# Performance work log

Hardware: AMD Instinct MI355X
Metric: run time of the kernel (lower is better)

Reference implementation:

```python
import jax, jax.numpy as jnp
import numpy as np

N_EMBD = 1024
N_HEAD = 16
B, T, T_MEM = 4, 1024, 1024


def setup_inputs() -> dict:
    key = jax.random.key(0)
    ks = jax.random.split(key, 11)
    s = 1.0 / np.sqrt(N_EMBD)
    return {
        "q_in": jax.random.normal(ks[0], (B, T, N_EMBD), jnp.float32),
        "k_in": jax.random.normal(ks[1], (B, T_MEM, N_EMBD), jnp.float32),
        "v_in": jax.random.normal(ks[2], (B, T_MEM, N_EMBD), jnp.float32),
        # torch nn.Linear weights: [out_features, in_features]
        "Wq": jax.random.normal(ks[3], (N_EMBD, N_EMBD), jnp.float32) * s,
        "bq": jax.random.normal(ks[4], (N_EMBD,), jnp.float32) * s,
        "Wk": jax.random.normal(ks[5], (N_EMBD, N_EMBD), jnp.float32) * s,
        "bk": jax.random.normal(ks[6], (N_EMBD,), jnp.float32) * s,
        "Wv": jax.random.normal(ks[7], (N_EMBD, N_EMBD), jnp.float32) * s,
        "bv": jax.random.normal(ks[8], (N_EMBD,), jnp.float32) * s,
        "Wo": jax.random.normal(ks[9], (N_EMBD, N_EMBD), jnp.float32) * s,
        "bo": jax.random.normal(ks[10], (N_EMBD,), jnp.float32) * s,
    }


def reference(q_in, k_in, v_in, Wq, bq, Wk, bk, Wv, bv, Wo, bo):
    b, t, c = q_in.shape
    t_mem = k_in.shape[1]
    hd = c // N_HEAD  # head dim

    def proj(x, W, bias):
        return x @ W.T + bias

    # [b, h, t, hd]
    q = proj(q_in, Wq, bq).reshape(b, t, N_HEAD, hd).transpose(0, 2, 1, 3)
    k = proj(k_in, Wk, bk).reshape(b, t_mem, N_HEAD, hd).transpose(0, 2, 1, 3)
    v = proj(v_in, Wv, bv).reshape(b, t_mem, N_HEAD, hd).transpose(0, 2, 1, 3)

    scale = 1.0 / np.sqrt(hd).astype(np.float32)
    att = jnp.einsum("bhqd,bhkd->bhqk", q, k) * scale
    att = jax.nn.softmax(att, axis=-1)  # dropout p=0 -> identity

    y = jnp.einsum("bhqk,bhkd->bhqd", att, v)
    y = y.transpose(0, 2, 1, 3).reshape(b, t, c)
    y = proj(y, Wo, bo)  # resid_drop p=0 -> identity

    attention = jnp.mean(att, axis=1)  # mean over heads: [b, t, t_mem]
    return (y, attention)
```

## Files before the change

kernel.cpp:

```cpp
#include <hip/hip_runtime.h>
#include <hip/hip_fp16.h>


typedef __attribute__((ext_vector_type(8))) short s16x8;
typedef __attribute__((ext_vector_type(4))) float f32x4;
typedef __attribute__((ext_vector_type(4))) unsigned short u16x4;

#define N_EMBD 1024
#define NH 16
#define BT 4096
#define STR 1032

#if __has_builtin(__builtin_amdgcn_global_load_lds)
#define HAVE_GLL 1
#define GLDS16(g, l)                                                              \
  __builtin_amdgcn_global_load_lds((__attribute__((address_space(1))) void*)(g), \
                                   (__attribute__((address_space(3))) void*)(l), 16, 0, 0)
#else
#define HAVE_GLL 0
#endif

static __device__ __forceinline__ unsigned short f2bf(float f) {
  unsigned int u = __builtin_bit_cast(unsigned int, f);
  u += 0x7FFFu + ((u >> 16) & 1u);
  return (unsigned short)(u >> 16);
}
static __device__ __forceinline__ float bf2f(unsigned short h) {
  return __builtin_bit_cast(float, ((unsigned int)h) << 16);
}

__global__ __launch_bounds__(256) void cvt_in3(const float* __restrict__ q,
                                               const float* __restrict__ k,
                                               const float* __restrict__ v,
                                               unsigned short* __restrict__ out) {
  const int z = blockIdx.z;
  const float* src = (z == 0) ? q : (z == 1 ? k : v);
  int i = (blockIdx.x * 256 + threadIdx.x) * 4;
  float4 val = *(const float4*)(src + i);
  u16x4 o;
  o[0] = f2bf(val.x);
  o[1] = f2bf(val.y);
  o[2] = f2bf(val.z);
  o[3] = f2bf(val.w);
  *(u16x4*)(out + (size_t)z * BT * N_EMBD + i) = o;
}

__global__ __launch_bounds__(256) void cvt_w4(const float* __restrict__ wo,
                                              const float* __restrict__ wq,
                                              const float* __restrict__ wk,
                                              const float* __restrict__ wv,
                                              unsigned short* __restrict__ out) {
  const int z = blockIdx.z;
  const float* src = (z == 0) ? wo : (z == 1 ? wq : (z == 2 ? wk : wv));
  const float scale = (z == 1) ? 0.125f : 1.0f;
  int i = (blockIdx.x * 256 + threadIdx.x) * 4;
  float4 val = *(const float4*)(src + i);
  u16x4 o;
  o[0] = f2bf(val.x * scale);
  o[1] = f2bf(val.y * scale);
  o[2] = f2bf(val.z * scale);
  o[3] = f2bf(val.w * scale);
  *(u16x4*)(out + (size_t)z * N_EMBD * N_EMBD + i) = o;
}

template <bool F32OUT>
static __device__ __forceinline__ void gemm_bt_tile(const unsigned short* __restrict__ A,
                                                    const unsigned short* __restrict__ B,
                                                    const float* __restrict__ bias, float bscale,
                                                    void* __restrict__ Cout,
                                                    int m0, int n0, int N, int K,
                                                    unsigned short* Al, unsigned short* Bl) {
  const int tid = threadIdx.x;
  const int l = tid & 63, w = tid >> 6;
  const int wr = w >> 1, wc = w & 1;
  const int l15 = l & 15, l4 = l >> 4;
  const int srow = tid >> 3;
  const int skk = (tid & 7) * 8;
  f32x4 acc[4][4] = {};
  for (int k0 = 0; k0 < K; k0 += 64) {
#if HAVE_GLL
#pragma unroll
    for (int i = 0; i < 4; ++i) {
      GLDS16(&A[(size_t)(m0 + i * 32 + srow) * K + k0 + skk], Al + i * 2048 + w * 512);
      GLDS16(&B[(size_t)(n0 + i * 32 + srow) * K + k0 + skk], Bl + i * 2048 + w * 512);
    }
#else
#pragma unroll
    for (int i = 0; i < 4; ++i) {
      int row = i * 32 + srow;
      *(s16x8*)&Al[row * 64 + skk] = *(const s16x8*)&A[(size_t)(m0 + row) * K + k0 + skk];
      *(s16x8*)&Bl[row * 64 + skk] = *(const s16x8*)&B[(size_t)(n0 + row) * K + k0 + skk];
    }
#endif
    __syncthreads();
#pragma unroll
    for (int kf = 0; kf < 2; ++kf) {
      s16x8 af[4], bfr[4];
#pragma unroll
      for (int mi = 0; mi < 4; ++mi)
        af[mi] = *(const s16x8*)&Al[(wr * 64 + mi * 16 + l15) * 64 + kf * 32 + l4 * 8];
#pragma unroll
      for (int nj = 0; nj < 4; ++nj)
        bfr[nj] = *(const s16x8*)&Bl[(wc * 64 + nj * 16 + l15) * 64 + kf * 32 + l4 * 8];
#pragma unroll
      for (int mi = 0; mi < 4; ++mi) {
#pragma unroll
        for (int nj = 0; nj < 4; ++nj)
          acc[mi][nj] =
              __builtin_amdgcn_mfma_f32_16x16x32_bf16(af[mi], bfr[nj], acc[mi][nj], 0, 0, 0);
      }
    }
    __syncthreads();
  }
#pragma unroll
  for (int nj = 0; nj < 4; ++nj) {
    int col = n0 + wc * 64 + nj * 16 + l15;
    float bv = bias[col] * bscale;
#pragma unroll
    for (int mi = 0; mi < 4; ++mi) {
#pragma unroll
      for (int r = 0; r < 4; ++r) {
        int row = m0 + wr * 64 + mi * 16 + l4 * 4 + r;
        float v = acc[mi][nj][r] + bv;
        if constexpr (F32OUT)
          ((float*)Cout)[(size_t)row * N + col] = v;
        else
          ((unsigned short*)Cout)[(size_t)row * N + col] = f2bf(v);
      }
    }
  }
}

__global__ __launch_bounds__(256) void gemm_qkv(const unsigned short* __restrict__ Xin,
                                                const unsigned short* __restrict__ Wbf,
                                                const float* __restrict__ bq,
                                                const float* __restrict__ bk,
                                                const float* __restrict__ bv,
                                                unsigned short* __restrict__ Cout) {
  __shared__ unsigned short Al[128 * 64];
  __shared__ unsigned short Bl[128 * 64];
  const int z = blockIdx.z;
  const float* bias = (z == 0) ? bq : (z == 1 ? bk : bv);
  const float bscale = (z == 0) ? 0.125f : 1.0f;
  gemm_bt_tile<false>(Xin + (size_t)z * BT * N_EMBD,
                      Wbf + (size_t)(1 + z) * N_EMBD * N_EMBD, bias, bscale,
                      Cout + (size_t)z * BT * N_EMBD, blockIdx.x * 128, blockIdx.y * 128,
                      N_EMBD, N_EMBD, Al, Bl);
}

__global__ __launch_bounds__(256) void gemm_out(const unsigned short* __restrict__ Ybf,
                                                const unsigned short* __restrict__ Wo,
                                                const float* __restrict__ bo,
                                                float* __restrict__ Cout) {
  __shared__ unsigned short Al[128 * 64];
  __shared__ unsigned short Bl[128 * 64];
  gemm_bt_tile<true>(Ybf, Wo, bo, 1.0f, Cout, blockIdx.x * 128, blockIdx.y * 128, N_EMBD, N_EMBD,
                     Al, Bl);
}

__global__ __launch_bounds__(256) void transpose_v(const unsigned short* __restrict__ Vp,
                                                   unsigned short* __restrict__ Vt) {
  __shared__ unsigned short tile[64][65];
  const int t0 = blockIdx.x * 64, h = blockIdx.y, b = blockIdx.z;
  const int r = threadIdx.x >> 2, c0 = (threadIdx.x & 3) * 16;
  const unsigned short* src = Vp + (size_t)(b * 1024 + t0 + r) * 1024 + h * 64 + c0;
#pragma unroll
  for (int j = 0; j < 16; ++j) tile[r][c0 + j] = src[j];
  __syncthreads();
  unsigned short* dst = Vt + (size_t)((b * 16 + h) * 64 + r) * 1024 + t0 + c0;
#pragma unroll
  for (int j = 0; j < 16; ++j) dst[j] = tile[c0 + j][r];
}

__global__ __launch_bounds__(512, 4) void attn_ph2(const unsigned short* __restrict__ Qp,
                                                   const unsigned short* __restrict__ Kp,
                                                   const unsigned short* __restrict__ Vt,
                                                   unsigned short* __restrict__ Ybf,
                                                   unsigned short* __restrict__ Pmean) {
  __shared__ __align__(16) unsigned short S2[2][16 * STR];
  __shared__ float RedM[2][16][4];
  __shared__ float RedS[2][16][4];
  const int tid = threadIdx.x;
  const int tm = tid >> 8;
  const int ttid = tid & 255;
  const int w4 = ttid >> 6;
  const int l = tid & 63;
  const int l15 = l & 15, l4 = l >> 4;
  const int r = ttid & 15, c = ttid >> 4;

  int bid = blockIdx.x;
  int swz = (bid & 7) * 64 + (bid >> 3);
  int qt = swz & 63;
  int grp = swz >> 6;
  int b = grp >> 1, hg = grp & 1;
  int q0 = qt * 16;

  __half2 am[32];
#pragma unroll
  for (int j = 0; j < 32; ++j) am[j] = __float2half2_rn(0.f);

#pragma unroll 1
  for (int it = 0; it < 4; ++it) {
    const int h = hg * 8 + it * 2 + tm;
    const unsigned short* qbase = Qp + (size_t)(b * 1024 + q0 + l15) * 1024 + h * 64 + l4 * 8;
    s16x8 aq0 = *(const s16x8*)qbase;
    s16x8 aq1 = *(const s16x8*)(qbase + 32);
    float m = -3.4e38f;
#pragma unroll
    for (int nt = 0; nt < 16; ++nt) {
      int gn = w4 * 16 + nt;
      const unsigned short* kb = Kp + (size_t)(b * 1024 + gn * 16 + l15) * 1024 + h * 64 + l4 * 8;
      f32x4 s = {};
      s = __builtin_amdgcn_mfma_f32_16x16x32_bf16(*(const s16x8*)kb, aq0, s, 0, 0, 0);
      s = __builtin_amdgcn_mfma_f32_16x16x32_bf16(*(const s16x8*)(kb + 32), aq1, s, 0, 0, 0);
      u16x4 pk;
#pragma unroll
      for (int rr = 0; rr < 4; ++rr) {
        m = fmaxf(m, s[rr]);
        pk[rr] = f2bf(s[rr]);
      }
      *(u16x4*)&S2[tm][l15 * STR + gn * 16 + l4 * 4] = pk;
    }
    m = fmaxf(m, __shfl_xor(m, 16));
    m = fmaxf(m, __shfl_xor(m, 32));
    if (l < 16) RedM[tm][l][w4] = m;
    __syncthreads();

    float mm = fmaxf(fmaxf(RedM[tm][r][0], RedM[tm][r][1]),
                     fmaxf(RedM[tm][r][2], RedM[tm][r][3]));
    float ps = 0.f;
#pragma unroll
    for (int k = 0; k < 8; ++k) {
      unsigned short* sp = &S2[tm][r * STR + c * 64 + k * 8];
      s16x8 sv = *(const s16x8*)sp;
      s16x8 pv;
#pragma unroll
      for (int j = 0; j < 8; ++j) {
        float e = __expf(bf2f((unsigned short)sv[j]) - mm);
        ps += e;
        pv[j] = (short)f2bf(e);
      }
      *(s16x8*)sp = pv;
    }
    ps += __shfl_xor(ps, 16);
    ps += __shfl_xor(ps, 32);
    if (l < 16) RedS[tm][l][w4] = ps;
    __syncthreads();

    float lsA = RedS[tm][l15][0] + RedS[tm][l15][1] + RedS[tm][l15][2] + RedS[tm][l15][3];
    float fac = 0.0625f / lsA;
    f32x4 y = {};
    const unsigned short* vb = Vt + (size_t)((b * 16 + h) * 64 + w4 * 16 + l15) * 1024 + l4 * 8;
#pragma unroll
    for (int kq = 0; kq < 4; ++kq) {
#pragma unroll
      for (int kk = 0; kk < 8; ++kk) {
        const int ks = kq * 8 + kk;
        s16x8 pa = *(const s16x8*)&S2[tm][l15 * STR + ks * 32 + l4 * 8];
        y = __builtin_amdgcn_mfma_f32_16x16x32_bf16(pa, *(const s16x8*)(vb + ks * 32), y, 0, 0, 0);
        if (kq == w4) {
#pragma unroll
          for (int e2 = 0; e2 < 4; ++e2) {
            float2 fv;
            fv.x = bf2f((unsigned short)pa[e2 * 2]) * fac;
            fv.y = bf2f((unsigned short)pa[e2 * 2 + 1]) * fac;
            am[kk * 4 + e2] = __hadd2(am[kk * 4 + e2], __float22half2_rn(fv));
          }
        }
      }
    }
#pragma unroll
    for (int rr = 0; rr < 4; ++rr) {
      int row = l4 * 4 + rr;
      float lsr = RedS[tm][row][0] + RedS[tm][row][1] + RedS[tm][row][2] + RedS[tm][row][3];
      Ybf[(size_t)(b * 1024 + q0 + row) * 1024 + h * 64 + w4 * 16 + l15] = f2bf(y[rr] / lsr);
    }
    __syncthreads();
  }

  unsigned int* us = (unsigned int*)S2;
  if (tm == 1) {
#pragma unroll
    for (int j = 0; j < 32; ++j) us[ttid * 32 + j] = __builtin_bit_cast(unsigned int, am[j]);
  }
  __syncthreads();
  if (tm == 0) {
    unsigned short* pm =
        Pmean + (size_t)((b * 2 + hg) * 1024 + q0 + l15) * 1024 + w4 * 256 + l4 * 8;
#pragma unroll
    for (int kk = 0; kk < 8; ++kk) {
      s16x8 ov;
#pragma unroll
      for (int e2 = 0; e2 < 4; ++e2) {
        int j = kk * 4 + e2;
        __half2 ot = __builtin_bit_cast(__half2, us[ttid * 32 + j]);
        float2 fo = __half22float2(ot);
        float2 fm = __half22float2(am[j]);
        ov[e2 * 2] = (short)f2bf(fm.x + fo.x);
        ov[e2 * 2 + 1] = (short)f2bf(fm.y + fo.y);
      }
      *(s16x8*)&pm[kk * 32] = ov;
    }
  }
}

__global__ __launch_bounds__(256) void mean2(const unsigned short* __restrict__ P2,
                                             float* __restrict__ out) {
  size_t f = ((size_t)blockIdx.x * 256 + threadIdx.x) * 8;
  int b = (int)(f >> 20);
  size_t i0 = f + ((size_t)b << 20);
  s16x8 a = *(const s16x8*)&P2[i0];
  s16x8 d = *(const s16x8*)&P2[i0 + (1u << 20)];
  float4 o0, o1;
  o0.x = bf2f((unsigned short)a[0]) + bf2f((unsigned short)d[0]);
  o0.y = bf2f((unsigned short)a[1]) + bf2f((unsigned short)d[1]);
  o0.z = bf2f((unsigned short)a[2]) + bf2f((unsigned short)d[2]);
  o0.w = bf2f((unsigned short)a[3]) + bf2f((unsigned short)d[3]);
  o1.x = bf2f((unsigned short)a[4]) + bf2f((unsigned short)d[4]);
  o1.y = bf2f((unsigned short)a[5]) + bf2f((unsigned short)d[5]);
  o1.z = bf2f((unsigned short)a[6]) + bf2f((unsigned short)d[6]);
  o1.w = bf2f((unsigned short)a[7]) + bf2f((unsigned short)d[7]);
  *(float4*)&out[f] = o0;
  *(float4*)&out[f + 4] = o1;
}

extern "C" void kernel_launch(void* const* d_in, const int* in_sizes, int n_in, void* d_out,
                              int out_size, void* d_ws, size_t ws_size, hipStream_t stream) {
  const float* q_in = (const float*)d_in[0];
  const float* k_in = (const float*)d_in[1];
  const float* v_in = (const float*)d_in[2];
  const float* Wq = (const float*)d_in[3];
  const float* bq = (const float*)d_in[4];
  const float* Wk = (const float*)d_in[5];
  const float* bk = (const float*)d_in[6];
  const float* Wv = (const float*)d_in[7];
  const float* bv = (const float*)d_in[8];
  const float* Wo = (const float*)d_in[9];
  const float* bo = (const float*)d_in[10];

  float* out_y = (float*)d_out;
  float* out_att = out_y + (size_t)BT * N_EMBD;

  char* ws = (char*)d_ws;
  const size_t MB = 1024 * 1024;
  unsigned short* xin_bf = (unsigned short*)(ws);
  unsigned short* W_bf = (unsigned short*)(ws + 24 * MB);
  unsigned short* Qp = (unsigned short*)(ws + 32 * MB);
  unsigned short* Kp = Qp + (size_t)BT * N_EMBD;
  unsigned short* Vp = Kp + (size_t)BT * N_EMBD;
  unsigned short* Pmean = (unsigned short*)(ws);
  unsigned short* Vt = (unsigned short*)(ws + 16 * MB);
  unsigned short* Ybf = Vp;

  const int NIN = BT * N_EMBD;
  const int NW = N_EMBD * N_EMBD;

  cvt_in3<<<dim3(NIN / 1024, 1, 3), 256, 0, stream>>>(q_in, k_in, v_in, xin_bf);
  cvt_w4<<<dim3(NW / 1024, 1, 4), 256, 0, stream>>>(Wo, Wq, Wk, Wv, W_bf);

  gemm_qkv<<<dim3(BT / 128, N_EMBD / 128, 3), 256, 0, stream>>>(xin_bf, W_bf, bq, bk, bv, Qp);
  transpose_v<<<dim3(16, 16, 4), 256, 0, stream>>>(Vp, Vt);
  attn_ph2<<<512, 512, 0, stream>>>(Qp, Kp, Vt, Ybf, Pmean);
  mean2<<<2048, 256, 0, stream>>>(Pmean, out_att);
  gemm_out<<<dim3(BT / 128, N_EMBD / 128), 256, 0, stream>>>(Ybf, W_bf, bo, out_y);
}
```

Measured before the change: 232.4 us.

## Double attention query tile to 32 rows per block with 1024-thread blocks

The attention kernel now processes 32 query rows per block instead of 16. Each loaded K fragment is reused for two query sub-tiles, and the block grows to 1024 threads with half as many blocks. This is meant to halve K global traffic per query row and amortise Q/K loads. In exchange the S2 scratch doubles to about 132 KB of LDS, which can limit occupancy to one block per CU. The grid shrinks to 256 blocks, and the block-index swizzle is replaced by a simpler mapping.

```diff
diff --git a/kernel.cpp b/kernel.cpp
--- a/kernel.cpp
+++ b/kernel.cpp
@@ -172,28 +172,28 @@
   for (int j = 0; j < 16; ++j) dst[j] = tile[c0 + j][r];
 }
 
-__global__ __launch_bounds__(512, 4) void attn_ph2(const unsigned short* __restrict__ Qp,
-                                                   const unsigned short* __restrict__ Kp,
-                                                   const unsigned short* __restrict__ Vt,
-                                                   unsigned short* __restrict__ Ybf,
-                                                   unsigned short* __restrict__ Pmean) {
-  __shared__ __align__(16) unsigned short S2[2][16 * STR];
-  __shared__ float RedM[2][16][4];
-  __shared__ float RedS[2][16][4];
+__global__ __launch_bounds__(1024, 4) void attn_ph2(const unsigned short* __restrict__ Qp,
+                                                    const unsigned short* __restrict__ Kp,
+                                                    const unsigned short* __restrict__ Vt,
+                                                    unsigned short* __restrict__ Ybf,
+                                                    unsigned short* __restrict__ Pmean) {
+  __shared__ __align__(16) unsigned short S2[2][32 * STR];
+  __shared__ float RedM[2][32][8];
+  __shared__ float RedS[2][32][8];
   const int tid = threadIdx.x;
-  const int tm = tid >> 8;
-  const int ttid = tid & 255;
+  const int tm = tid >> 9;
+  const int ttid = tid & 511;
   const int w4 = ttid >> 6;
   const int l = tid & 63;
   const int l15 = l & 15, l4 = l >> 4;
-  const int r = ttid & 15, c = ttid >> 4;
-
-  int bid = blockIdx.x;
-  int swz = (bid & 7) * 64 + (bid >> 3);
-  int qt = swz & 63;
-  int grp = swz >> 6;
-  int b = grp >> 1, hg = grp & 1;
-  int q0 = qt * 16;
+  const int r = ttid & 31, c = ttid >> 5;
+  const int qgw = w4 >> 2;
+  const int dtw = w4 & 3;
+
+  const int bid = blockIdx.x;
+  const int grp = bid & 7, qt = bid >> 3;
+  const int b = grp >> 1, hg = grp & 1;
+  const int q0 = qt * 32;
 
   __half2 am[32];
 #pragma unroll
@@ -202,32 +202,48 @@
 #pragma unroll 1
   for (int it = 0; it < 4; ++it) {
     const int h = hg * 8 + it * 2 + tm;
-    const unsigned short* qbase = Qp + (size_t)(b * 1024 + q0 + l15) * 1024 + h * 64 + l4 * 8;
-    s16x8 aq0 = *(const s16x8*)qbase;
-    s16x8 aq1 = *(const s16x8*)(qbase + 32);
-    float m = -3.4e38f;
-#pragma unroll
-    for (int nt = 0; nt < 16; ++nt) {
-      int gn = w4 * 16 + nt;
+    const unsigned short* qb0 = Qp + (size_t)(b * 1024 + q0 + l15) * 1024 + h * 64 + l4 * 8;
+    const unsigned short* qb1 = qb0 + (size_t)16 * 1024;
+    s16x8 aq00 = *(const s16x8*)qb0;
+    s16x8 aq01 = *(const s16x8*)(qb0 + 32);
+    s16x8 aq10 = *(const s16x8*)qb1;
+    s16x8 aq11 = *(const s16x8*)(qb1 + 32);
+    float m0 = -3.4e38f, m1 = -3.4e38f;
+#pragma unroll
+    for (int nt = 0; nt < 8; ++nt) {
+      int gn = w4 * 8 + nt;
       const unsigned short* kb = Kp + (size_t)(b * 1024 + gn * 16 + l15) * 1024 + h * 64 + l4 * 8;
-      f32x4 s = {};
-      s = __builtin_amdgcn_mfma_f32_16x16x32_bf16(*(const s16x8*)kb, aq0, s, 0, 0, 0);
-      s = __builtin_amdgcn_mfma_f32_16x16x32_bf16(*(const s16x8*)(kb + 32), aq1, s, 0, 0, 0);
-      u16x4 pk;
+      s16x8 kf0 = *(const s16x8*)kb;
+      s16x8 kf1 = *(const s16x8*)(kb + 32);
+      f32x4 s0 = {}, s1 = {};
+      s0 = __builtin_amdgcn_mfma_f32_16x16x32_bf16(kf0, aq00, s0, 0, 0, 0);
+      s0 = __builtin_amdgcn_mfma_f32_16x16x32_bf16(kf1, aq01, s0, 0, 0, 0);
+      s1 = __builtin_amdgcn_mfma_f32_16x16x32_bf16(kf0, aq10, s1, 0, 0, 0);
+      s1 = __builtin_amdgcn_mfma_f32_16x16x32_bf16(kf1, aq11, s1, 0, 0, 0);
+      u16x4 p0, p1;
 #pragma unroll
       for (int rr = 0; rr < 4; ++rr) {
-        m = fmaxf(m, s[rr]);
-        pk[rr] = f2bf(s[rr]);
-      }
-      *(u16x4*)&S2[tm][l15 * STR + gn * 16 + l4 * 4] = pk;
-    }
-    m = fmaxf(m, __shfl_xor(m, 16));
-    m = fmaxf(m, __shfl_xor(m, 32));
-    if (l < 16) RedM[tm][l][w4] = m;
-    __syncthreads();
-
-    float mm = fmaxf(fmaxf(RedM[tm][r][0], RedM[tm][r][1]),
-                     fmaxf(RedM[tm][r][2], RedM[tm][r][3]));
+        m0 = fmaxf(m0, s0[rr]);
+        p0[rr] = f2bf(s0[rr]);
+        m1 = fmaxf(m1, s1[rr]);
+        p1[rr] = f2bf(s1[rr]);
+      }
+      *(u16x4*)&S2[tm][l15 * STR + gn * 16 + l4 * 4] = p0;
+      *(u16x4*)&S2[tm][(16 + l15) * STR + gn * 16 + l4 * 4] = p1;
+    }
+    m0 = fmaxf(m0, __shfl_xor(m0, 16));
+    m0 = fmaxf(m0, __shfl_xor(m0, 32));
+    m1 = fmaxf(m1, __shfl_xor(m1, 16));
+    m1 = fmaxf(m1, __shfl_xor(m1, 32));
+    if (l < 16) {
+      RedM[tm][l][w4] = m0;
+      RedM[tm][16 + l][w4] = m1;
+    }
+    __syncthreads();
+
+    float mm = RedM[tm][r][0];
+#pragma unroll
+    for (int j = 1; j < 8; ++j) mm = fmaxf(mm, RedM[tm][r][j]);
     float ps = 0.f;
 #pragma unroll
     for (int k = 0; k < 8; ++k) {
@@ -242,23 +258,25 @@
       }
       *(s16x8*)sp = pv;
     }
-    ps += __shfl_xor(ps, 16);
     ps += __shfl_xor(ps, 32);
-    if (l < 16) RedS[tm][l][w4] = ps;
-    __syncthreads();
-
-    float lsA = RedS[tm][l15][0] + RedS[tm][l15][1] + RedS[tm][l15][2] + RedS[tm][l15][3];
+    if (l < 32) RedS[tm][l][w4] = ps;
+    __syncthreads();
+
+    float lsA = 0.f;
+#pragma unroll
+    for (int j = 0; j < 8; ++j) lsA += RedS[tm][qgw * 16 + l15][j];
     float fac = 0.0625f / lsA;
     f32x4 y = {};
-    const unsigned short* vb = Vt + (size_t)((b * 16 + h) * 64 + w4 * 16 + l15) * 1024 + l4 * 8;
+    const unsigned short* vb =
+        Vt + (size_t)((b * 16 + h) * 64 + dtw * 16 + l15) * 1024 + l4 * 8;
 #pragma unroll
     for (int kq = 0; kq < 4; ++kq) {
 #pragma unroll
       for (int kk = 0; kk < 8; ++kk) {
         const int ks = kq * 8 + kk;
-        s16x8 pa = *(const s16x8*)&S2[tm][l15 * STR + ks * 32 + l4 * 8];
+        s16x8 pa = *(const s16x8*)&S2[tm][(qgw * 16 + l15) * STR + ks * 32 + l4 * 8];
         y = __builtin_amdgcn_mfma_f32_16x16x32_bf16(pa, *(const s16x8*)(vb + ks * 32), y, 0, 0, 0);
-        if (kq == w4) {
+        if (kq == dtw) {
 #pragma unroll
           for (int e2 = 0; e2 < 4; ++e2) {
             float2 fv;
@@ -271,9 +289,11 @@
     }
 #pragma unroll
     for (int rr = 0; rr < 4; ++rr) {
-      int row = l4 * 4 + rr;
-      float lsr = RedS[tm][row][0] + RedS[tm][row][1] + RedS[tm][row][2] + RedS[tm][row][3];
-      Ybf[(size_t)(b * 1024 + q0 + row) * 1024 + h * 64 + w4 * 16 + l15] = f2bf(y[rr] / lsr);
+      int row = qgw * 16 + l4 * 4 + rr;
+      float lsr = 0.f;
+#pragma unroll
+      for (int j = 0; j < 8; ++j) lsr += RedS[tm][row][j];
+      Ybf[(size_t)(b * 1024 + q0 + row) * 1024 + h * 64 + dtw * 16 + l15] = f2bf(y[rr] / lsr);
     }
     __syncthreads();
   }
@@ -285,8 +305,8 @@
   }
   __syncthreads();
   if (tm == 0) {
-    unsigned short* pm =
-        Pmean + (size_t)((b * 2 + hg) * 1024 + q0 + l15) * 1024 + w4 * 256 + l4 * 8;
+    unsigned short* pm = Pmean + ((size_t)(b * 2 + hg) << 20) +
+                         (size_t)(q0 + qgw * 16 + l15) * 1024 + dtw * 256 + l4 * 8;
 #pragma unroll
     for (int kk = 0; kk < 8; ++kk) {
       s16x8 ov;
@@ -360,7 +380,7 @@
 
   gemm_qkv<<<dim3(BT / 128, N_EMBD / 128, 3), 256, 0, stream>>>(xin_bf, W_bf, bq, bk, bv, Qp);
   transpose_v<<<dim3(16, 16, 4), 256, 0, stream>>>(Vp, Vt);
-  attn_ph2<<<512, 512, 0, stream>>>(Qp, Kp, Vt, Ybf, Pmean);
+  attn_ph2<<<256, 1024, 0, stream>>>(Qp, Kp, Vt, Ybf, Pmean);
   mean2<<<2048, 256, 0, stream>>>(Pmean, out_att);
   gemm_out<<<dim3(BT / 128, N_EMBD / 128), 256, 0, stream>>>(Ybf, W_bf, bo, out_y);
 }
```

Result: faster. 222.2 us (-4.4%).

## Double attention query tile per block and keep scores in registers before softmax

Applied to the files above, without the earlier changes.

The attention kernel now handles 32 query rows per block with 1024 threads instead of 16 rows with 512, halving the grid. Each wave keeps its QK^T scores in registers, takes the row max, then exponentiates and writes bf16 probabilities to shared memory only once. This removes the bf16 round trip of raw scores through LDS and packs with v_cvt_pk_bf16_f32. It also raises wave priority around the MFMA loops. The costs are a larger LDS footprint and more register pressure per block, fewer blocks per CU, and a dropped block-index swizzle that may change L2 locality.

```diff
diff --git a/kernel.cpp b/kernel.cpp
--- a/kernel.cpp
+++ b/kernel.cpp
@@ -172,28 +172,29 @@
   for (int j = 0; j < 16; ++j) dst[j] = tile[c0 + j][r];
 }
 
-__global__ __launch_bounds__(512, 4) void attn_ph2(const unsigned short* __restrict__ Qp,
-                                                   const unsigned short* __restrict__ Kp,
-                                                   const unsigned short* __restrict__ Vt,
-                                                   unsigned short* __restrict__ Ybf,
-                                                   unsigned short* __restrict__ Pmean) {
-  __shared__ __align__(16) unsigned short S2[2][16 * STR];
-  __shared__ float RedM[2][16][4];
-  __shared__ float RedS[2][16][4];
+__global__ __launch_bounds__(1024, 4) void attn_ph2(const unsigned short* __restrict__ Qp,
+                                                    const unsigned short* __restrict__ Kp,
+                                                    const unsigned short* __restrict__ Vt,
+                                                    unsigned short* __restrict__ Ybf,
+                                                    unsigned short* __restrict__ Pmean) {
+  __shared__ __align__(16) unsigned short S2[2][32 * STR];
+  __shared__ float RedM[2][32][8];
+  __shared__ float RedS[2][32][4];
   const int tid = threadIdx.x;
-  const int tm = tid >> 8;
-  const int ttid = tid & 255;
+  const int tm = tid >> 9;
+  const int ttid = tid & 511;
   const int w4 = ttid >> 6;
   const int l = tid & 63;
   const int l15 = l & 15, l4 = l >> 4;
-  const int r = ttid & 15, c = ttid >> 4;
-
-  int bid = blockIdx.x;
-  int swz = (bid & 7) * 64 + (bid >> 3);
-  int qt = swz & 63;
-  int grp = swz >> 6;
-  int b = grp >> 1, hg = grp & 1;
-  int q0 = qt * 16;
+  const int qg = w4 & 1;
+  const int gnr = w4 >> 1;
+  const int qgw = w4 >> 2;
+  const int dtw = w4 & 3;
+
+  const int bid = blockIdx.x;
+  const int grp = bid & 7, qt = bid >> 3;
+  const int b = grp >> 1, hg = grp & 1;
+  const int q0 = qt * 32;
 
   __half2 am[32];
 #pragma unroll
@@ -202,63 +203,70 @@
 #pragma unroll 1
   for (int it = 0; it < 4; ++it) {
     const int h = hg * 8 + it * 2 + tm;
-    const unsigned short* qbase = Qp + (size_t)(b * 1024 + q0 + l15) * 1024 + h * 64 + l4 * 8;
+    const unsigned short* qbase =
+        Qp + (size_t)(b * 1024 + q0 + qg * 16 + l15) * 1024 + h * 64 + l4 * 8;
     s16x8 aq0 = *(const s16x8*)qbase;
     s16x8 aq1 = *(const s16x8*)(qbase + 32);
+    f32x4 sacc[16];
     float m = -3.4e38f;
+    __builtin_amdgcn_s_setprio(1);
 #pragma unroll
     for (int nt = 0; nt < 16; ++nt) {
-      int gn = w4 * 16 + nt;
+      int gn = gnr * 16 + nt;
       const unsigned short* kb = Kp + (size_t)(b * 1024 + gn * 16 + l15) * 1024 + h * 64 + l4 * 8;
       f32x4 s = {};
       s = __builtin_amdgcn_mfma_f32_16x16x32_bf16(*(const s16x8*)kb, aq0, s, 0, 0, 0);
       s = __builtin_amdgcn_mfma_f32_16x16x32_bf16(*(const s16x8*)(kb + 32), aq1, s, 0, 0, 0);
-      u16x4 pk;
-#pragma unroll
-      for (int rr = 0; rr < 4; ++rr) {
-        m = fmaxf(m, s[rr]);
-        pk[rr] = f2bf(s[rr]);
-      }
-      *(u16x4*)&S2[tm][l15 * STR + gn * 16 + l4 * 4] = pk;
-    }
+      sacc[nt] = s;
+#pragma unroll
+      for (int rr = 0; rr < 4; ++rr) m = fmaxf(m, s[rr]);
+    }
+    __builtin_amdgcn_s_setprio(0);
     m = fmaxf(m, __shfl_xor(m, 16));
     m = fmaxf(m, __shfl_xor(m, 32));
-    if (l < 16) RedM[tm][l][w4] = m;
-    __syncthreads();
-
-    float mm = fmaxf(fmaxf(RedM[tm][r][0], RedM[tm][r][1]),
-                     fmaxf(RedM[tm][r][2], RedM[tm][r][3]));
+    if (l < 16) RedM[tm][qg * 16 + l][w4] = m;
+    __syncthreads();
+
+    const int row = qg * 16 + l15;
+    float mm = RedM[tm][row][0];
+#pragma unroll
+    for (int j = 1; j < 8; ++j) mm = fmaxf(mm, RedM[tm][row][j]);
     float ps = 0.f;
 #pragma unroll
-    for (int k = 0; k < 8; ++k) {
-      unsigned short* sp = &S2[tm][r * STR + c * 64 + k * 8];
-      s16x8 sv = *(const s16x8*)sp;
-      s16x8 pv;
-#pragma unroll
-      for (int j = 0; j < 8; ++j) {
-        float e = __expf(bf2f((unsigned short)sv[j]) - mm);
-        ps += e;
-        pv[j] = (short)f2bf(e);
-      }
-      *(s16x8*)sp = pv;
+    for (int nt = 0; nt < 16; ++nt) {
+      float e0 = __expf(sacc[nt][0] - mm);
+      float e1 = __expf(sacc[nt][1] - mm);
+      float e2 = __expf(sacc[nt][2] - mm);
+      float e3 = __expf(sacc[nt][3] - mm);
+      ps += (e0 + e1) + (e2 + e3);
+      unsigned int lo, hi;
+      asm("v_cvt_pk_bf16_f32 %0, %1, %2" : "=v"(lo) : "v"(e0), "v"(e1));
+      asm("v_cvt_pk_bf16_f32 %0, %1, %2" : "=v"(hi) : "v"(e2), "v"(e3));
+      uint2 pk;
+      pk.x = lo;
+      pk.y = hi;
+      *(uint2*)&S2[tm][row * STR + (gnr * 16 + nt) * 16 + l4 * 4] = pk;
     }
     ps += __shfl_xor(ps, 16);
     ps += __shfl_xor(ps, 32);
-    if (l < 16) RedS[tm][l][w4] = ps;
-    __syncthreads();
-
-    float lsA = RedS[tm][l15][0] + RedS[tm][l15][1] + RedS[tm][l15][2] + RedS[tm][l15][3];
+    if (l < 16) RedS[tm][qg * 16 + l][gnr] = ps;
+    __syncthreads();
+
+    float lsA = RedS[tm][qgw * 16 + l15][0] + RedS[tm][qgw * 16 + l15][1] +
+                RedS[tm][qgw * 16 + l15][2] + RedS[tm][qgw * 16 + l15][3];
     float fac = 0.0625f / lsA;
     f32x4 y = {};
-    const unsigned short* vb = Vt + (size_t)((b * 16 + h) * 64 + w4 * 16 + l15) * 1024 + l4 * 8;
+    const unsigned short* vb =
+        Vt + (size_t)((b * 16 + h) * 64 + dtw * 16 + l15) * 1024 + l4 * 8;
+    __builtin_amdgcn_s_setprio(1);
 #pragma unroll
     for (int kq = 0; kq < 4; ++kq) {
 #pragma unroll
       for (int kk = 0; kk < 8; ++kk) {
         const int ks = kq * 8 + kk;
-        s16x8 pa = *(const s16x8*)&S2[tm][l15 * STR + ks * 32 + l4 * 8];
+        s16x8 pa = *(const s16x8*)&S2[tm][(qgw * 16 + l15) * STR + ks * 32 + l4 * 8];
         y = __builtin_amdgcn_mfma_f32_16x16x32_bf16(pa, *(const s16x8*)(vb + ks * 32), y, 0, 0, 0);
-        if (kq == w4) {
+        if (kq == dtw) {
 #pragma unroll
           for (int e2 = 0; e2 < 4; ++e2) {
             float2 fv;
@@ -269,11 +277,12 @@
         }
       }
     }
+    __builtin_amdgcn_s_setprio(0);
 #pragma unroll
     for (int rr = 0; rr < 4; ++rr) {
-      int row = l4 * 4 + rr;
-      float lsr = RedS[tm][row][0] + RedS[tm][row][1] + RedS[tm][row][2] + RedS[tm][row][3];
-      Ybf[(size_t)(b * 1024 + q0 + row) * 1024 + h * 64 + w4 * 16 + l15] = f2bf(y[rr] / lsr);
+      int row2 = qgw * 16 + l4 * 4 + rr;
+      float lsr = RedS[tm][row2][0] + RedS[tm][row2][1] + RedS[tm][row2][2] + RedS[tm][row2][3];
+      Ybf[(size_t)(b * 1024 + q0 + row2) * 1024 + h * 64 + dtw * 16 + l15] = f2bf(y[rr] / lsr);
     }
     __syncthreads();
   }
@@ -285,8 +294,8 @@
   }
   __syncthreads();
   if (tm == 0) {
-    unsigned short* pm =
-        Pmean + (size_t)((b * 2 + hg) * 1024 + q0 + l15) * 1024 + w4 * 256 + l4 * 8;
+    unsigned short* pm = Pmean + ((size_t)(b * 2 + hg) << 20) +
+                         (size_t)(q0 + qgw * 16 + l15) * 1024 + dtw * 256 + l4 * 8;
 #pragma unroll
     for (int kk = 0; kk < 8; ++kk) {
       s16x8 ov;
@@ -360,7 +369,7 @@
 
   gemm_qkv<<<dim3(BT / 128, N_EMBD / 128, 3), 256, 0, stream>>>(xin_bf, W_bf, bq, bk, bv, Qp);
   transpose_v<<<dim3(16, 16, 4), 256, 0, stream>>>(Vp, Vt);
-  attn_ph2<<<512, 512, 0, stream>>>(Qp, Kp, Vt, Ybf, Pmean);
+  attn_ph2<<<256, 1024, 0, stream>>>(Qp, Kp, Vt, Ybf, Pmean);
   mean2<<<2048, 256, 0, stream>>>(Pmean, out_att);
   gemm_out<<<dim3(BT / 128, N_EMBD / 128), 256, 0, stream>>>(Ybf, W_bf, bo, out_y);
 }
```

After: 244.8 us. 1.05x slower.
